# Kernel optimization log

Hardware: AMD Instinct MI355X
Metric: run time of the kernel (lower is better)

Reference implementation:

```python
import jax, jax.numpy as jnp
import numpy as np

DIM = 64
M_DIM = 16
EDGE_DIM = 0
IN_DIM = 2 * DIM + EDGE_DIM + 1  # 129


def _mlp(x, W1, b1, W2, b2):
    return jax.nn.relu(x @ W1 + b1) @ W2 + b2


def setup_inputs() -> dict:
    key = jax.random.key(0)
    ks = jax.random.split(key, 10)
    s = 0.02
    inp = {
        "feats": jax.random.normal(ks[0], (1, 1024, DIM), dtype=jnp.float32),
        "coors": jax.random.normal(ks[1], (1, 1024, 3), dtype=jnp.float32),
        # edge_mlp: Linear(129,258) -> ReLU -> Linear(258,16)
        "eW1": jax.random.normal(ks[2], (IN_DIM, IN_DIM * 2), dtype=jnp.float32) * s,
        "eb1": jnp.zeros((IN_DIM * 2,), jnp.float32),
        "eW2": jax.random.normal(ks[3], (IN_DIM * 2, M_DIM), dtype=jnp.float32) * s,
        "eb2": jnp.zeros((M_DIM,), jnp.float32),
        # coors_mlp: Linear(16,64) -> ReLU -> Linear(64,1)
        "cW1": jax.random.normal(ks[4], (M_DIM, M_DIM * 4), dtype=jnp.float32) * s,
        "cb1": jnp.zeros((M_DIM * 4,), jnp.float32),
        "cW2": jax.random.normal(ks[5], (M_DIM * 4, 1), dtype=jnp.float32) * s,
        "cb2": jnp.zeros((1,), jnp.float32),
        # hidden_mlp: Linear(80,128) -> ReLU -> Linear(128,64)
        "hW1": jax.random.normal(ks[6], (DIM + M_DIM, DIM * 2), dtype=jnp.float32) * s,
        "hb1": jnp.zeros((DIM * 2,), jnp.float32),
        "hW2": jax.random.normal(ks[7], (DIM * 2, DIM), dtype=jnp.float32) * s,
        "hb2": jnp.zeros((DIM,), jnp.float32),
    }
    return inp


def reference(feats, coors, eW1, eb1, eW2, eb2, cW1, cb1, cW2, cb2, hW1, hb1, hW2, hb2):
    b, n, d = feats.shape
    # all-pairs relative coordinates and distances: (b, n, n, 3), (b, n, n, 1)
    rel_coors = coors[:, :, None, :] - coors[:, None, :, :]
    rel_dist = jnp.linalg.norm(rel_coors, axis=-1, keepdims=True)
    feats_i = jnp.broadcast_to(feats[:, :, None, :], (b, n, n, d))
    feats_j = jnp.broadcast_to(feats[:, None, :, :], (b, n, n, d))
    edge_input = jnp.concatenate([feats_i, feats_j, rel_dist], axis=-1)  # (b,n,n,2d+1)
    m_ij = _mlp(edge_input, eW1, eb1, eW2, eb2)                          # (b,n,n,m_dim)
    coor_weights = _mlp(m_ij, cW1, cb1, cW2, cb2)[..., 0]                # (b,n,n)
    coors_out = jnp.einsum('bij,bijc->bic', coor_weights, rel_coors)     # (b,n,3)
    m_i = m_ij.sum(axis=-2)                                              # (b,n,m_dim)
    hidden_out = _mlp(jnp.concatenate([feats, m_i], axis=-1), hW1, hb1, hW2, hb2)
    return (hidden_out, coors_out)
```

## Files before the change

### kernel.cpp

```cpp
#include <hip/hip_runtime.h>
#include <hip/hip_bf16.h>
#include <stdint.h>

#define N 1024
#define DIM 64
#define MDIM 16
#define EH 258
#define EHP 264
#define CH 64
#define HH 128
#define PRE_ROWS 8

typedef __bf16 bf16x8 __attribute__((ext_vector_type(8)));
typedef float f32x4 __attribute__((ext_vector_type(4)));
typedef float f32x2 __attribute__((ext_vector_type(2)));
typedef uint32_t u32x4 __attribute__((ext_vector_type(4)));
union B8 { uint32_t u[4]; bf16x8 v; };

__device__ __forceinline__ uint32_t cvtpk(float lo, float hi) {
  uint32_t r;
  asm("v_cvt_pk_bf16_f32 %0, %1, %2" : "=v"(r) : "v"(lo), "v"(hi));
  return r;
}
__device__ __forceinline__ f32x2 pk_add(f32x2 a, f32x2 b) {
  f32x2 r;
  asm("v_pk_add_f32 %0, %1, %2" : "=v"(r) : "v"(a), "v"(b));
  return r;
}
__device__ __forceinline__ f32x2 pk_fma(f32x2 a, f32x2 b, f32x2 c) {
  f32x2 r;
  asm("v_pk_fma_f32 %0, %1, %2, %3" : "=v"(r) : "v"(a), "v"(b), "v"(c));
  return r;
}
__device__ __forceinline__ float bflo(uint32_t u) { return __uint_as_float(u << 16); }
__device__ __forceinline__ float bfhi(uint32_t u) { return __uint_as_float(u & 0xffff0000u); }

__global__ __launch_bounds__(256) void eg_pre(
    const float* __restrict__ feats, const float* __restrict__ eW1,
    const float* __restrict__ eb1,
    float* __restrict__ A, __hip_bfloat16* __restrict__ Bb)
{
  __shared__ float sf[PRE_ROWS][DIM];
  int ib = blockIdx.x, t = threadIdx.x;
  for (int q = t; q < PRE_ROWS * DIM; q += 256)
    sf[q >> 6][q & 63] = feats[ib * PRE_ROWS * DIM + q];
  __syncthreads();
  for (int k = t; k < EH; k += 256) {
    float bias = eb1[k];
    float a[PRE_ROWS], bv[PRE_ROWS];
#pragma unroll
    for (int ii = 0; ii < PRE_ROWS; ++ii) { a[ii] = bias; bv[ii] = 0.f; }
#pragma unroll 4
    for (int d = 0; d < DIM; ++d) {
      float wt = eW1[d * EH + k];
      float wb = eW1[(DIM + d) * EH + k];
#pragma unroll
      for (int ii = 0; ii < PRE_ROWS; ++ii) {
        a[ii]  = fmaf(sf[ii][d], wt, a[ii]);
        bv[ii] = fmaf(sf[ii][d], wb, bv[ii]);
      }
    }
#pragma unroll
    for (int ii = 0; ii < PRE_ROWS; ++ii) {
      A[(ib * PRE_ROWS + ii) * EH + k] = a[ii];
      Bb[(ib * PRE_ROWS + ii) * EHP + k] = __float2bfloat16(bv[ii]);
    }
  }
}

__global__ __launch_bounds__(256, 2) void eg_main(
    const float* __restrict__ feats, const float* __restrict__ coors,
    const float* __restrict__ eW1, const float* __restrict__ eW2,
    const float* __restrict__ eb2, const float* __restrict__ cW1,
    const float* __restrict__ cb1, const float* __restrict__ cW2,
    const float* __restrict__ cb2, const float* __restrict__ hW1,
    const float* __restrict__ hb1, const float* __restrict__ hW2,
    const float* __restrict__ hb2,
    const float* __restrict__ A, const __hip_bfloat16* __restrict__ Bb,
    float* __restrict__ out)
{
  __shared__ __align__(16) float sA[EHP];
  __shared__ __align__(16) float sW3[EHP];
  __shared__ __align__(16) float4 sRel4[N];
  __shared__ __align__(16) float sCB1[CH];
  __shared__ __align__(16) float sCW2[CH];
  __shared__ float sEB2[MDIM], sFeat[DIM];
  __shared__ struct { float redm[4][16]; float redc[4][3]; float mi[MDIM]; float hid[HH]; } sE;

  const int i = blockIdx.x, t = threadIdx.x;
  const int lane = t & 63, wv = t >> 6;
  const int r16 = lane & 15, g = lane >> 4;

  for (int q = t; q < EH; q += 256) { sA[q] = A[i * EH + q]; sW3[q] = eW1[128 * EH + q]; }
  if (t < CH)   { sCB1[t] = cb1[t]; sCW2[t] = cW2[t]; }
  if (t < MDIM) sEB2[t] = eb2[t];
  if (t < DIM)  sFeat[t] = feats[i * DIM + t];
  {
    float cx = coors[i * 3], cy = coors[i * 3 + 1], cz = coors[i * 3 + 2];
    const float4* c4 = (const float4*)coors;
    float4 ca = c4[t * 3 + 0], cb = c4[t * 3 + 1], cc = c4[t * 3 + 2];
    float jx[4] = {ca.x, ca.w, cb.z, cc.y};
    float jy[4] = {ca.y, cb.x, cb.w, cc.z};
    float jz[4] = {ca.z, cb.y, cc.x, cc.w};
#pragma unroll
    for (int q = 0; q < 4; ++q) {
      float rx = cx - jx[q], ry = cy - jy[q], rz = cz - jz[q];
      float d = sqrtf(fmaf(rx, rx, fmaf(ry, ry, rz * rz)));
      sRel4[t * 4 + q] = make_float4(rx, ry, rz, d);
    }
  }

  B8 few[8];
#pragma unroll
  for (int s = 0; s < 8; ++s) {
    const float* ew = eW2 + (s * 32 + g * 8) * MDIM + r16;
    float fe[8];
#pragma unroll
    for (int e = 0; e < 8; ++e) fe[e] = ew[e * MDIM];
    few[s].u[0] = cvtpk(fe[0], fe[1]); few[s].u[1] = cvtpk(fe[2], fe[3]);
    few[s].u[2] = cvtpk(fe[4], fe[5]); few[s].u[3] = cvtpk(fe[6], fe[7]);
  }
  B8 fcw1[4];
#pragma unroll
  for (int T = 0; T < 4; ++T) {
    float cv[8];
#pragma unroll
    for (int e = 0; e < 8; ++e)
      cv[e] = (g < 2) ? cW1[(8 * g + e) * CH + 16 * T + r16] : 0.f;
    fcw1[T].u[0] = cvtpk(cv[0], cv[1]); fcw1[T].u[1] = cvtpk(cv[2], cv[3]);
    fcw1[T].u[2] = cvtpk(cv[4], cv[5]); fcw1[T].u[3] = cvtpk(cv[6], cv[7]);
  }
  float tw0[4], tw1[4];
#pragma unroll
  for (int r = 0; r < 4; ++r) {
    tw0[r] = eW2[256 * MDIM + 4 * g + r];
    tw1[r] = eW2[257 * MDIM + 4 * g + r];
  }
  float cb2v = cb2[0];
  __syncthreads();

  f32x4 eb2r;
#pragma unroll
  for (int r = 0; r < 4; ++r) eb2r[r] = sEB2[4 * g + r];
  float a256 = sA[256], a257 = sA[257], w356 = sW3[256], w357 = sW3[257];

  const f32x2* sA2 = (const f32x2*)sA;
  const f32x2* sW32 = (const f32x2*)sW3;
  const char* Bbyte = (const char*)Bb;

  float macc[4] = {0.f, 0.f, 0.f, 0.f};
  float cax = 0.f, cay = 0.f, caz = 0.f;

#pragma unroll 1
  for (int p = 0; p < 2; ++p) {
    const int jb = wv * 16 + p * 512;
    float djp[8];
    f32x4 D[8];
    const char* brow[8];
#pragma unroll
    for (int tt = 0; tt < 8; ++tt) {
      djp[tt] = sRel4[jb + tt * 64 + r16].w;
      D[tt] = eb2r;
      brow[tt] = Bbyte + (size_t)((jb + tt * 64 + r16) * (EHP * 2) + g * 16);
    }

#pragma unroll
    for (int s = 0; s < 8; ++s) {
      f32x2 a2[4], w2[4];
#pragma unroll
      for (int q = 0; q < 4; ++q) {
        a2[q] = sA2[16 * s + 4 * g + q];
        w2[q] = sW32[16 * s + 4 * g + q];
      }
#pragma unroll
      for (int tt = 0; tt < 8; ++tt) {
        u32x4 bq = *(const u32x4*)(brow[tt] + s * 64);
        f32x2 dd; dd[0] = djp[tt]; dd[1] = djp[tt];
        B8 hb;
#pragma unroll
        for (int q = 0; q < 4; ++q) {
          f32x2 bp; bp[0] = bflo(bq[q]); bp[1] = bfhi(bq[q]);
          f32x2 hv = pk_add(bp, a2[q]);
          hv = pk_fma(dd, w2[q], hv);
          hb.u[q] = cvtpk(fmaxf(hv[0], 0.f), fmaxf(hv[1], 0.f));
        }
        D[tt] = __builtin_amdgcn_mfma_f32_16x16x32_bf16(few[s].v, hb.v, D[tt], 0, 0, 0);
      }
    }

    const f32x4* cb14 = (const f32x4*)sCB1;
    const f32x4* cw24 = (const f32x4*)sCW2;
#pragma unroll
    for (int tt = 0; tt < 8; ++tt) {
      const int j = jb + tt * 64 + r16;
      float4 rl = sRel4[j];
      uint32_t bt = *(const uint32_t*)(Bbyte + (size_t)(j * (EHP * 2) + 512));
      float h6 = fmaxf(fmaf(rl.w, w356, a256 + bflo(bt)), 0.f);
      float h7 = fmaxf(fmaf(rl.w, w357, a257 + bfhi(bt)), 0.f);
#pragma unroll
      for (int r = 0; r < 4; ++r) {
        D[tt][r] = fmaf(h6, tw0[r], D[tt][r]);
        D[tt][r] = fmaf(h7, tw1[r], D[tt][r]);
        macc[r] += D[tt][r];
      }
      uint32_t p0 = cvtpk(D[tt][0], D[tt][1]);
      uint32_t p1 = cvtpk(D[tt][2], D[tt][3]);
      int s0 = r16 + (((2 * g) & 3) << 4);
      int s1 = r16 + (((2 * g + 1) & 3) << 4);
      uint32_t b0 = (uint32_t)__shfl((int)p0, s0, 64);
      uint32_t b1 = (uint32_t)__shfl((int)p1, s0, 64);
      uint32_t b2 = (uint32_t)__shfl((int)p0, s1, 64);
      uint32_t b3 = (uint32_t)__shfl((int)p1, s1, 64);
      B8 mf;
      mf.u[0] = (g < 2) ? b0 : 0u; mf.u[1] = (g < 2) ? b1 : 0u;
      mf.u[2] = (g < 2) ? b2 : 0u; mf.u[3] = (g < 2) ? b3 : 0u;
      float wacc = 0.f;
#pragma unroll
      for (int T = 0; T < 4; ++T) {
        f32x4 cbv = cb14[4 * T + g];
        f32x4 hd = __builtin_amdgcn_mfma_f32_16x16x32_bf16(fcw1[T].v, mf.v, cbv, 0, 0, 0);
        f32x4 cwv = cw24[4 * T + g];
#pragma unroll
        for (int r = 0; r < 4; ++r)
          wacc = fmaf(fmaxf(hd[r], 0.f), cwv[r], wacc);
      }
      wacc += __shfl_xor(wacc, 16, 64);
      wacc += __shfl_xor(wacc, 32, 64);
      float w = cb2v + wacc;
      cax = fmaf(w, rl.x, cax); cay = fmaf(w, rl.y, cay); caz = fmaf(w, rl.z, caz);
    }
  }

#pragma unroll
  for (int off = 1; off < 16; off <<= 1) {
#pragma unroll
    for (int r = 0; r < 4; ++r) macc[r] += __shfl_xor(macc[r], off, 64);
    cax += __shfl_xor(cax, off, 64);
    cay += __shfl_xor(cay, off, 64);
    caz += __shfl_xor(caz, off, 64);
  }
  if (r16 == 0) {
#pragma unroll
    for (int r = 0; r < 4; ++r) sE.redm[wv][4 * g + r] = macc[r];
    if (g == 0) { sE.redc[wv][0] = cax; sE.redc[wv][1] = cay; sE.redc[wv][2] = caz; }
  }
  __syncthreads();
  if (t < MDIM)
    sE.mi[t] = sE.redm[0][t] + sE.redm[1][t] + sE.redm[2][t] + sE.redm[3][t];
  if (t >= 16 && t < 19) {
    int c = t - 16;
    out[N * DIM + i * 3 + c] = sE.redc[0][c] + sE.redc[1][c] + sE.redc[2][c] + sE.redc[3][c];
  }
  __syncthreads();

  if (t < HH) {
    float acc = hb1[t];
#pragma unroll 8
    for (int d = 0; d < DIM; ++d) acc = fmaf(sFeat[d], hW1[d * HH + t], acc);
#pragma unroll
    for (int d = 0; d < MDIM; ++d) acc = fmaf(sE.mi[d], hW1[(DIM + d) * HH + t], acc);
    sE.hid[t] = fmaxf(acc, 0.f);
  }
  __syncthreads();
  if (t < DIM) {
    float acc = hb2[t];
#pragma unroll 8
    for (int c = 0; c < HH; ++c) acc = fmaf(sE.hid[c], hW2[c * DIM + t], acc);
    out[i * DIM + t] = acc;
  }
}

extern "C" void kernel_launch(void* const* d_in, const int* in_sizes, int n_in,
                              void* d_out, int out_size, void* d_ws, size_t ws_size,
                              hipStream_t stream) {
  const float* feats = (const float*)d_in[0];
  const float* coors = (const float*)d_in[1];
  const float* eW1   = (const float*)d_in[2];
  const float* eb1   = (const float*)d_in[3];
  const float* eW2   = (const float*)d_in[4];
  const float* eb2   = (const float*)d_in[5];
  const float* cW1   = (const float*)d_in[6];
  const float* cb1   = (const float*)d_in[7];
  const float* cW2   = (const float*)d_in[8];
  const float* cb2   = (const float*)d_in[9];
  const float* hW1   = (const float*)d_in[10];
  const float* hb1   = (const float*)d_in[11];
  const float* hW2   = (const float*)d_in[12];
  const float* hb2   = (const float*)d_in[13];

  float* A = (float*)d_ws;
  __hip_bfloat16* Bb = (__hip_bfloat16*)((char*)d_ws + (size_t)N * EH * 4);
  float* out = (float*)d_out;

  eg_pre<<<N / PRE_ROWS, 256, 0, stream>>>(feats, eW1, eb1, A, Bb);
  eg_main<<<N, 256, 0, stream>>>(feats, coors, eW1, eW2, eb2, cW1, cb1, cW2, cb2,
                                 hW1, hb1, hW2, hb2, A, Bb, out);
}
```

Measured before the change: 164.0 us.

## Split per-node edge kernel into single-wave quarter blocks plus post kernel

The 256-thread per-node block, where four waves each handle a slice of neighbors, becomes 4N single-wave blocks, each covering a quarter (256) of the neighbors. Partial message sums and coordinate sums go to a workspace buffer, and a new post kernel reduces them and runs the hidden MLP. This removes block-level syncs and the serial hidden-MLP tail from the main kernel, and should give finer scheduling granularity and better occupancy. In exchange it adds a third launch, a global round trip for the partials, and repeated per-block setup: each small block reloads the weight fragments and shared data.

```diff
diff --git a/kernel.cpp b/kernel.cpp
--- a/kernel.cpp
+++ b/kernel.cpp
@@ -10,6 +10,7 @@
 #define CH 64
 #define HH 128
 #define PRE_ROWS 8
+#define QN 256
 
 typedef __bf16 bf16x8 __attribute__((ext_vector_type(8)));
 typedef float f32x4 __attribute__((ext_vector_type(4)));
@@ -68,45 +69,43 @@
   }
 }
 
-__global__ __launch_bounds__(256, 2) void eg_main(
-    const float* __restrict__ feats, const float* __restrict__ coors,
-    const float* __restrict__ eW1, const float* __restrict__ eW2,
-    const float* __restrict__ eb2, const float* __restrict__ cW1,
-    const float* __restrict__ cb1, const float* __restrict__ cW2,
-    const float* __restrict__ cb2, const float* __restrict__ hW1,
-    const float* __restrict__ hb1, const float* __restrict__ hW2,
-    const float* __restrict__ hb2,
+__global__ __launch_bounds__(64, 3) void eg_quarter(
+    const float* __restrict__ coors, const float* __restrict__ eW1,
+    const float* __restrict__ eW2, const float* __restrict__ eb2,
+    const float* __restrict__ cW1, const float* __restrict__ cb1,
+    const float* __restrict__ cW2, const float* __restrict__ cb2,
     const float* __restrict__ A, const __hip_bfloat16* __restrict__ Bb,
-    float* __restrict__ out)
+    float* __restrict__ part)
 {
   __shared__ __align__(16) float sA[EHP];
   __shared__ __align__(16) float sW3[EHP];
-  __shared__ __align__(16) float4 sRel4[N];
+  __shared__ __align__(16) float4 sRel4[QN];
   __shared__ __align__(16) float sCB1[CH];
   __shared__ __align__(16) float sCW2[CH];
-  __shared__ float sEB2[MDIM], sFeat[DIM];
-  __shared__ struct { float redm[4][16]; float redc[4][3]; float mi[MDIM]; float hid[HH]; } sE;
-
-  const int i = blockIdx.x, t = threadIdx.x;
-  const int lane = t & 63, wv = t >> 6;
+  __shared__ float sEB2[MDIM];
+
+  const int bid = blockIdx.x;
+  const int i = bid >> 2, q = bid & 3;
+  const int lane = threadIdx.x;
   const int r16 = lane & 15, g = lane >> 4;
 
-  for (int q = t; q < EH; q += 256) { sA[q] = A[i * EH + q]; sW3[q] = eW1[128 * EH + q]; }
-  if (t < CH)   { sCB1[t] = cb1[t]; sCW2[t] = cW2[t]; }
-  if (t < MDIM) sEB2[t] = eb2[t];
-  if (t < DIM)  sFeat[t] = feats[i * DIM + t];
+  for (int k = lane; k < EH; k += 64) { sA[k] = A[i * EH + k]; sW3[k] = eW1[128 * EH + k]; }
+  sCB1[lane] = cb1[lane];
+  sCW2[lane] = cW2[lane];
+  if (lane < MDIM) sEB2[lane] = eb2[lane];
   {
     float cx = coors[i * 3], cy = coors[i * 3 + 1], cz = coors[i * 3 + 2];
     const float4* c4 = (const float4*)coors;
-    float4 ca = c4[t * 3 + 0], cb = c4[t * 3 + 1], cc = c4[t * 3 + 2];
+    int base = q * 192 + lane * 3;
+    float4 ca = c4[base], cb = c4[base + 1], cc = c4[base + 2];
     float jx[4] = {ca.x, ca.w, cb.z, cc.y};
     float jy[4] = {ca.y, cb.x, cb.w, cc.z};
     float jz[4] = {ca.z, cb.y, cc.x, cc.w};
 #pragma unroll
-    for (int q = 0; q < 4; ++q) {
-      float rx = cx - jx[q], ry = cy - jy[q], rz = cz - jz[q];
+    for (int qq = 0; qq < 4; ++qq) {
+      float rx = cx - jx[qq], ry = cy - jy[qq], rz = cz - jz[qq];
       float d = sqrtf(fmaf(rx, rx, fmaf(ry, ry, rz * rz)));
-      sRel4[t * 4 + q] = make_float4(rx, ry, rz, d);
+      sRel4[lane * 4 + qq] = make_float4(rx, ry, rz, d);
     }
   }
 
@@ -152,25 +151,26 @@
   float cax = 0.f, cay = 0.f, caz = 0.f;
 
 #pragma unroll 1
-  for (int p = 0; p < 2; ++p) {
-    const int jb = wv * 16 + p * 512;
+  for (int P = 0; P < 2; ++P) {
+    const int jlb = P * 128;
     float djp[8];
     f32x4 D[8];
     const char* brow[8];
 #pragma unroll
     for (int tt = 0; tt < 8; ++tt) {
-      djp[tt] = sRel4[jb + tt * 64 + r16].w;
+      const int jl = jlb + tt * 16 + r16;
+      djp[tt] = sRel4[jl].w;
       D[tt] = eb2r;
-      brow[tt] = Bbyte + (size_t)((jb + tt * 64 + r16) * (EHP * 2) + g * 16);
+      brow[tt] = Bbyte + (size_t)((q * QN + jl) * (EHP * 2) + g * 16);
     }
 
 #pragma unroll
     for (int s = 0; s < 8; ++s) {
       f32x2 a2[4], w2[4];
 #pragma unroll
-      for (int q = 0; q < 4; ++q) {
-        a2[q] = sA2[16 * s + 4 * g + q];
-        w2[q] = sW32[16 * s + 4 * g + q];
+      for (int qq = 0; qq < 4; ++qq) {
+        a2[qq] = sA2[16 * s + 4 * g + qq];
+        w2[qq] = sW32[16 * s + 4 * g + qq];
       }
 #pragma unroll
       for (int tt = 0; tt < 8; ++tt) {
@@ -178,11 +178,11 @@
         f32x2 dd; dd[0] = djp[tt]; dd[1] = djp[tt];
         B8 hb;
 #pragma unroll
-        for (int q = 0; q < 4; ++q) {
-          f32x2 bp; bp[0] = bflo(bq[q]); bp[1] = bfhi(bq[q]);
-          f32x2 hv = pk_add(bp, a2[q]);
-          hv = pk_fma(dd, w2[q], hv);
-          hb.u[q] = cvtpk(fmaxf(hv[0], 0.f), fmaxf(hv[1], 0.f));
+        for (int qq = 0; qq < 4; ++qq) {
+          f32x2 bp; bp[0] = bflo(bq[qq]); bp[1] = bfhi(bq[qq]);
+          f32x2 hv = pk_add(bp, a2[qq]);
+          hv = pk_fma(dd, w2[qq], hv);
+          hb.u[qq] = cvtpk(fmaxf(hv[0], 0.f), fmaxf(hv[1], 0.f));
         }
         D[tt] = __builtin_amdgcn_mfma_f32_16x16x32_bf16(few[s].v, hb.v, D[tt], 0, 0, 0);
       }
@@ -192,9 +192,9 @@
     const f32x4* cw24 = (const f32x4*)sCW2;
 #pragma unroll
     for (int tt = 0; tt < 8; ++tt) {
-      const int j = jb + tt * 64 + r16;
-      float4 rl = sRel4[j];
-      uint32_t bt = *(const uint32_t*)(Bbyte + (size_t)(j * (EHP * 2) + 512));
+      const int jl = jlb + tt * 16 + r16;
+      float4 rl = sRel4[jl];
+      uint32_t bt = *(const uint32_t*)(Bbyte + (size_t)((q * QN + jl) * (EHP * 2) + 512));
       float h6 = fmaxf(fmaf(rl.w, w356, a256 + bflo(bt)), 0.f);
       float h7 = fmaxf(fmaf(rl.w, w357, a257 + bfhi(bt)), 0.f);
 #pragma unroll
@@ -240,32 +240,42 @@
     caz += __shfl_xor(caz, off, 64);
   }
   if (r16 == 0) {
-#pragma unroll
-    for (int r = 0; r < 4; ++r) sE.redm[wv][4 * g + r] = macc[r];
-    if (g == 0) { sE.redc[wv][0] = cax; sE.redc[wv][1] = cay; sE.redc[wv][2] = caz; }
+    float* pp = part + bid * 20;
+#pragma unroll
+    for (int r = 0; r < 4; ++r) pp[4 * g + r] = macc[r];
+    if (g == 0) { pp[16] = cax; pp[17] = cay; pp[18] = caz; }
+  }
+}
+
+__global__ __launch_bounds__(128) void eg_post(
+    const float* __restrict__ feats, const float* __restrict__ part,
+    const float* __restrict__ hW1, const float* __restrict__ hb1,
+    const float* __restrict__ hW2, const float* __restrict__ hb2,
+    float* __restrict__ out)
+{
+  __shared__ float sFeat[DIM], sMi[MDIM], sHid[HH];
+  const int i = blockIdx.x, t = threadIdx.x;
+  if (t < DIM) sFeat[t] = feats[i * DIM + t];
+  if (t < 19) {
+    const float* pp = part + i * 4 * 20;
+    float v = pp[t] + pp[20 + t] + pp[40 + t] + pp[60 + t];
+    if (t < MDIM) sMi[t] = v;
+    else out[N * DIM + i * 3 + (t - MDIM)] = v;
   }
   __syncthreads();
-  if (t < MDIM)
-    sE.mi[t] = sE.redm[0][t] + sE.redm[1][t] + sE.redm[2][t] + sE.redm[3][t];
-  if (t >= 16 && t < 19) {
-    int c = t - 16;
-    out[N * DIM + i * 3 + c] = sE.redc[0][c] + sE.redc[1][c] + sE.redc[2][c] + sE.redc[3][c];
-  }
-  __syncthreads();
-
-  if (t < HH) {
+  {
     float acc = hb1[t];
 #pragma unroll 8
     for (int d = 0; d < DIM; ++d) acc = fmaf(sFeat[d], hW1[d * HH + t], acc);
 #pragma unroll
-    for (int d = 0; d < MDIM; ++d) acc = fmaf(sE.mi[d], hW1[(DIM + d) * HH + t], acc);
-    sE.hid[t] = fmaxf(acc, 0.f);
+    for (int d = 0; d < MDIM; ++d) acc = fmaf(sMi[d], hW1[(DIM + d) * HH + t], acc);
+    sHid[t] = fmaxf(acc, 0.f);
   }
   __syncthreads();
   if (t < DIM) {
     float acc = hb2[t];
 #pragma unroll 8
-    for (int c = 0; c < HH; ++c) acc = fmaf(sE.hid[c], hW2[c * DIM + t], acc);
+    for (int c = 0; c < HH; ++c) acc = fmaf(sHid[c], hW2[c * DIM + t], acc);
     out[i * DIM + t] = acc;
   }
 }
@@ -288,11 +298,14 @@
   const float* hW2   = (const float*)d_in[12];
   const float* hb2   = (const float*)d_in[13];
 
-  float* A = (float*)d_ws;
-  __hip_bfloat16* Bb = (__hip_bfloat16*)((char*)d_ws + (size_t)N * EH * 4);
+  char* ws = (char*)d_ws;
+  float* A = (float*)ws;
+  __hip_bfloat16* Bb = (__hip_bfloat16*)(ws + (size_t)N * EH * 4);
+  float* part = (float*)(ws + (size_t)N * EH * 4 + (size_t)N * EHP * 2);
   float* out = (float*)d_out;
 
   eg_pre<<<N / PRE_ROWS, 256, 0, stream>>>(feats, eW1, eb1, A, Bb);
-  eg_main<<<N, 256, 0, stream>>>(feats, coors, eW1, eW2, eb2, cW1, cb1, cW2, cb2,
-                                 hW1, hb1, hW2, hb2, A, Bb, out);
-}
+  eg_quarter<<<4 * N, 64, 0, stream>>>(coors, eW1, eW2, eb2, cW1, cb1, cW2, cb2,
+                                       A, Bb, part);
+  eg_post<<<N, HH, 0, stream>>>(feats, part, hW1, hb1, hW2, hb2, out);
+}
```

Result: slower. 211.1 us (+28.7%).
